# Optimization experiments

Measured on AMD Instinct MI355X. Metric: run time of the kernel, lower is better.

## Reference

```python
import jax, jax.numpy as jnp
import numpy as np

EMBED_DIM = 256
NUM_EMBEDDINGS = 1024
COMMITMENT_COST = 0.25


def setup_inputs() -> dict:
    key = jax.random.key(0)
    k1, k2 = jax.random.split(key)
    z_e = jax.random.normal(k1, (64, 32, 32, EMBED_DIM), dtype=jnp.float32)
    # variance_scaling(fan_in, uniform) ~ U(-sqrt(3/fan_in), sqrt(3/fan_in))
    lim = float(np.sqrt(3.0 / EMBED_DIM))
    codebook = jax.random.uniform(k2, (NUM_EMBEDDINGS, EMBED_DIM), dtype=jnp.float32,
                                  minval=-lim, maxval=lim)
    return {"z_e": z_e, "codebook": codebook}


def reference(z_e, codebook):
    codebook = jnp.asarray(codebook, dtype=jnp.float32)
    z_flat = jnp.reshape(z_e, (-1, codebook.shape[1]))  # [N, D]
    # ||z||^2 - 2 z.c + ||c||^2 -> [N, K]
    distances = (jnp.sum(z_flat ** 2, axis=1, keepdims=True)
                 - 2.0 * jnp.dot(z_flat, codebook.T)
                 + jnp.sum(codebook ** 2, axis=1))
    encoding_indices = jnp.argmin(distances, axis=1)  # [N]
    quantized = jnp.reshape(codebook[encoding_indices], z_e.shape)
    commitment_loss = COMMITMENT_COST * jnp.mean((jax.lax.stop_gradient(quantized) - z_e) ** 2)
    embedding_loss = jnp.mean((quantized - jax.lax.stop_gradient(z_e)) ** 2)
    quantized = z_e + jax.lax.stop_gradient(quantized - z_e)  # straight-through
    return (quantized, commitment_loss, embedding_loss, encoding_indices)
```

## Files before the change

kernel.cpp:

```cpp
#include <hip/hip_runtime.h>

#define NROWS  65536
#define DIM    256
#define KCB    1024
#define DELTA  0.012f
#define DELTA2 2.0e-4f
#define NRMAX  65536

typedef __attribute__((ext_vector_type(8))) _Float16 v8h;
typedef __attribute__((ext_vector_type(4))) float v4f;
typedef __attribute__((ext_vector_type(4))) int   v4i;

__device__ __forceinline__ unsigned short h16(float x) {
  _Float16 h = (_Float16)x;
  return __builtin_bit_cast(unsigned short, h);
}
__device__ __forceinline__ unsigned pk2h(float a, float b) {
  return (unsigned)h16(a) | ((unsigned)h16(b) << 16);
}
__device__ __forceinline__ v4i pk8h(float4 a, float4 b) {
  v4i r; r.x = (int)pk2h(a.x,a.y); r.y = (int)pk2h(a.z,a.w);
  r.z = (int)pk2h(b.x,b.y); r.w = (int)pk2h(b.z,b.w);
  return r;
}
__device__ __forceinline__ float f16f(float x) { return (float)(_Float16)x; }
__device__ __forceinline__ void gld16(const void* g, void* l) {
  __builtin_amdgcn_global_load_lds(
      (const __attribute__((address_space(1))) unsigned int*)g,
      (__attribute__((address_space(3))) unsigned int*)l, 16, 0, 0);
}

__global__ __launch_bounds__(256) void prep_kernel(const float* __restrict__ cb,
                                                   float* __restrict__ cnorm,
                                                   unsigned short* __restrict__ cbh,
                                                   unsigned short* __restrict__ cbl,
                                                   int* __restrict__ cnt,
                                                   int* __restrict__ cnt2) {
  int g = blockIdx.x * 256 + threadIdx.x;
  if (g == 0) { *cnt = 0; *cnt2 = 0; }
  int k = g >> 2, q = g & 3;
  int nt = k >> 7, c = k & 127;
  const float4* row = reinterpret_cast<const float4*>(cb + (size_t)k * DIM) + q * 16;
  size_t off = (size_t)((nt * 4 + q) * 128 + c) * 64;
  unsigned short* dh = cbh + off;
  unsigned short* dl = cbl + off;
  int xr = (c & 7) << 3;
  double s = 0.0;
#pragma unroll
  for (int i = 0; i < 8; ++i) {
    float4 a = row[2 * i], b = row[2 * i + 1];
    s += (double)a.x * a.x + (double)a.y * a.y + (double)a.z * a.z + (double)a.w * a.w;
    s += (double)b.x * b.x + (double)b.y * b.y + (double)b.z * b.z + (double)b.w * b.w;
    *(v4i*)(dh + ((i * 8) ^ xr)) = pk8h(a, b);
    float4 ar, br;
    ar.x = a.x - f16f(a.x); ar.y = a.y - f16f(a.y);
    ar.z = a.z - f16f(a.z); ar.w = a.w - f16f(a.w);
    br.x = b.x - f16f(b.x); br.y = b.y - f16f(b.y);
    br.z = b.z - f16f(b.z); br.w = b.w - f16f(b.w);
    *(v4i*)(dl + ((i * 8) ^ xr)) = pk8h(ar, br);
  }
  s += __shfl_xor(s, 1);
  s += __shfl_xor(s, 2);
  if (q == 0) cnorm[k] = (float)s;
}

__global__ __launch_bounds__(256, 2) void vq_mfma(
    const float* __restrict__ z, const unsigned short* __restrict__ cbh,
    const float* __restrict__ cnw, int* __restrict__ idx_arr,
    int* __restrict__ list, int* __restrict__ cnt) {
  __shared__ __align__(16) short S[32768];

  const int t = threadIdx.x;
  const int l = t & 63;
  const int w = t >> 6;
  const int l15 = l & 15, lhi = l >> 4;
  const int wm = w * 32;
  const int r0 = blockIdx.x * 128;

#pragma unroll
  for (int p = 0; p < 16; ++p) {
    int u = t + p * 256;
    int row = u >> 5, k8 = u & 31;
    const float4* s = (const float4*)(z + (size_t)(r0 + row) * DIM + k8 * 8);
    float4 a = s[0], b = s[1];
    *(v4i*)(S + row * 256 + ((k8 * 8) ^ ((row & 7) << 3))) = pk8h(a, b);
  }
  __syncthreads();

  v8h A[2][8];
#pragma unroll
  for (int mf = 0; mf < 2; ++mf) {
    int arow = wm + mf * 16 + l15;
    int base = arow * 256, xr = (arow & 7) << 3;
#pragma unroll
    for (int ks8 = 0; ks8 < 8; ++ks8)
      A[mf][ks8] = *(const v8h*)(S + base + ((ks8 * 32 + lhi * 8) ^ xr));
  }
  float cn4[4];
#pragma unroll
  for (int j = 0; j < 4; ++j) cn4[j] = cnw[t + j * 256];
  __syncthreads();

  float* CNS = (float*)(S + 24576);
#pragma unroll
  for (int j = 0; j < 4; ++j) CNS[t + j * 256] = cn4[j];

  auto stageC = [&](int g) {
    const char* gb = (const char*)cbh + (size_t)g * 16384 + w * 4096 + l * 16;
    char* lb = (char*)S + (g % 3) * 16384 + w * 4096 + l * 16;
#pragma unroll
    for (int j = 0; j < 4; ++j) gld16(gb + j * 1024, lb + j * 1024);
  };

  int bcode[8], boff[8], bxr[8];
#pragma unroll
  for (int nf = 0; nf < 8; ++nf) {
    bcode[nf] = nf * 16 + l15;
    boff[nf] = bcode[nf] * 64;
    bxr[nf] = (bcode[nf] & 7) << 3;
  }

  float m1[8], m2[8]; int i1[8];
#pragma unroll
  for (int sl = 0; sl < 8; ++sl) { m1[sl] = 3.0e38f; m2[sl] = 3.0e38f; i1[sl] = 0; }

  __syncthreads();
  stageC(0); stageC(1);

  v4f acc[2][8];

  for (int nt = 0; nt < 8; ++nt) {
#pragma unroll
    for (int mf = 0; mf < 2; ++mf)
#pragma unroll
      for (int nf = 0; nf < 8; ++nf) acc[mf][nf] = (v4f){0.f, 0.f, 0.f, 0.f};

    for (int kc = 0; kc < 4; ++kc) {
      int g = nt * 4 + kc;
      if (g < 31) asm volatile("s_waitcnt vmcnt(4)" ::: "memory");
      else        asm volatile("s_waitcnt vmcnt(0)" ::: "memory");
      __builtin_amdgcn_s_barrier();
      __builtin_amdgcn_sched_barrier(0);
      if (g + 2 < 32) stageC(g + 2);
      const short* cur = S + (g % 3) * 8192;
#pragma unroll
      for (int ks = 0; ks < 2; ++ks) {
        int ko = ks * 32 + lhi * 8;
        v8h b[8];
#pragma unroll
        for (int nf = 0; nf < 8; ++nf)
          b[nf] = *(const v8h*)(cur + boff[nf] + (ko ^ bxr[nf]));
#pragma unroll
        for (int mf = 0; mf < 2; ++mf)
#pragma unroll
          for (int nf = 0; nf < 8; ++nf)
            acc[mf][nf] = __builtin_amdgcn_mfma_f32_16x16x32_f16(A[mf][kc * 2 + ks], b[nf], acc[mf][nf], 0, 0, 0);
      }
    }

#pragma unroll
    for (int mf = 0; mf < 2; ++mf)
#pragma unroll
      for (int nf = 0; nf < 8; ++nf) {
        int code = nt * 128 + bcode[nf];
        float cn = CNS[nt * 128 + bcode[nf]];
#pragma unroll
        for (int r = 0; r < 4; ++r) {
          float s = fmaf(-2.f, acc[mf][nf][r], cn);
          int sl = mf * 4 + r;
          m2[sl] = fminf(m2[sl], fmaxf(m1[sl], s));
          bool lt = s < m1[sl];
          i1[sl] = lt ? code : i1[sl];
          m1[sl] = lt ? s : m1[sl];
        }
      }
  }

#pragma unroll
  for (int off = 1; off < 16; off <<= 1) {
#pragma unroll
    for (int sl = 0; sl < 8; ++sl) {
      float o1 = __shfl_xor(m1[sl], off);
      int   oi = __shfl_xor(i1[sl], off);
      float o2 = __shfl_xor(m2[sl], off);
      bool bb = (o1 < m1[sl]) || (o1 == m1[sl] && oi < i1[sl]);
      float hi = fmaxf(m1[sl], o1);
      m2[sl] = fminf(hi, fminf(m2[sl], o2));
      m1[sl] = bb ? o1 : m1[sl];
      i1[sl] = bb ? oi : i1[sl];
    }
  }

  if (l15 == 0) {
#pragma unroll
    for (int sl = 0; sl < 8; ++sl) {
      int row = wm + (sl >> 2) * 16 + lhi * 4 + (sl & 3);
      idx_arr[r0 + row] = i1[sl];
      if (m2[sl] - m1[sl] < DELTA) {
        int p = atomicAdd(cnt, 1);
        list[p] = r0 + row;
      }
    }
  }
}

__global__ __launch_bounds__(256, 1) void vq_refine(
    const float* __restrict__ z,
    const unsigned short* __restrict__ cbh, const unsigned short* __restrict__ cbl,
    const float* __restrict__ cnw, const int* __restrict__ list,
    const int* __restrict__ cnt,
    float* __restrict__ pm1, float* __restrict__ pm2, int* __restrict__ pi1) {
  __shared__ __align__(16) short Ch[2][8192];
  __shared__ __align__(16) short Cl[2][8192];
  __shared__ int rows_s[64];

  const int t = threadIdx.x;
  const int l = t & 63, w = t >> 6;
  const int l15 = l & 15, lhi = l >> 4;
  const int n = *cnt;
  const int ngroups = (n + 63) >> 6;
  const int cq = blockIdx.x & 3;

  auto stage2 = [&](int g, int buf) {
    size_t go = (size_t)g * 16384 + w * 4096 + l * 16;
    char* lh = (char*)Ch[buf] + w * 4096;
    char* ll = (char*)Cl[buf] + w * 4096;
#pragma unroll
    for (int j = 0; j < 4; ++j) gld16((const char*)cbh + go + j * 1024, lh + j * 1024);
#pragma unroll
    for (int j = 0; j < 4; ++j) gld16((const char*)cbl + go + j * 1024, ll + j * 1024);
  };

  const int bxr = (l15 & 7) << 3;

  for (int grp = blockIdx.x >> 2; grp < ngroups; grp += (gridDim.x >> 2)) {
    int base = grp * 64;
    __syncthreads();
    if (t < 64) rows_s[t] = list[min(base + t, n - 1)];
    __syncthreads();
    int rowg = rows_s[w * 16 + l15];

    v8h Ah[8], Al[8];
#pragma unroll
    for (int ks8 = 0; ks8 < 8; ++ks8) {
      const float* p = z + (size_t)rowg * 256 + ks8 * 32 + lhi * 8;
      float4 a = *(const float4*)p, b = *(const float4*)(p + 4);
      v8h hv, lv;
      hv[0] = (_Float16)a.x; lv[0] = (_Float16)(a.x - (float)hv[0]);
      hv[1] = (_Float16)a.y; lv[1] = (_Float16)(a.y - (float)hv[1]);
      hv[2] = (_Float16)a.z; lv[2] = (_Float16)(a.z - (float)hv[2]);
      hv[3] = (_Float16)a.w; lv[3] = (_Float16)(a.w - (float)hv[3]);
      hv[4] = (_Float16)b.x; lv[4] = (_Float16)(b.x - (float)hv[4]);
      hv[5] = (_Float16)b.y; lv[5] = (_Float16)(b.y - (float)hv[5]);
      hv[6] = (_Float16)b.z; lv[6] = (_Float16)(b.z - (float)hv[6]);
      hv[7] = (_Float16)b.w; lv[7] = (_Float16)(b.w - (float)hv[7]);
      Ah[ks8] = hv; Al[ks8] = lv;
    }

    stage2(cq * 8, 0);
    __syncthreads();

    float m1[4], m2[4]; int i1[4];
#pragma unroll
    for (int r = 0; r < 4; ++r) { m1[r] = 3.0e38f; m2[r] = 3.0e38f; i1[r] = 0; }

#pragma unroll
    for (int tnt = 0; tnt < 2; ++tnt) {
      int nt = cq * 2 + tnt;
      float cnv[8];
#pragma unroll
      for (int nf = 0; nf < 8; ++nf) cnv[nf] = cnw[nt * 128 + nf * 16 + l15];

      v4f acc[8];
#pragma unroll
      for (int nf = 0; nf < 8; ++nf) acc[nf] = (v4f){0.f, 0.f, 0.f, 0.f};

      for (int kc = 0; kc < 4; ++kc) {
        int ph = tnt * 4 + kc;
        int g = nt * 4 + kc;
        if (ph < 7) stage2(g + 1, (ph + 1) & 1);
        const short* ch = Ch[ph & 1];
        const short* cl = Cl[ph & 1];
#pragma unroll
        for (int ks = 0; ks < 2; ++ks) {
          int ko = (ks * 32 + lhi * 8) ^ bxr;
          v8h bh[8], bl8[8];
#pragma unroll
          for (int nf = 0; nf < 8; ++nf) {
            int bo = (nf * 16 + l15) * 64 + ko;
            bh[nf]  = *(const v8h*)(ch + bo);
            bl8[nf] = *(const v8h*)(cl + bo);
          }
          v8h ah = Ah[kc * 2 + ks], al = Al[kc * 2 + ks];
#pragma unroll
          for (int nf = 0; nf < 8; ++nf) {
            acc[nf] = __builtin_amdgcn_mfma_f32_16x16x32_f16(al, bh[nf], acc[nf], 0, 0, 0);
            acc[nf] = __builtin_amdgcn_mfma_f32_16x16x32_f16(ah, bl8[nf], acc[nf], 0, 0, 0);
            acc[nf] = __builtin_amdgcn_mfma_f32_16x16x32_f16(ah, bh[nf], acc[nf], 0, 0, 0);
          }
        }
        __syncthreads();
      }

#pragma unroll
      for (int nf = 0; nf < 8; ++nf) {
        int code = nt * 128 + nf * 16 + l15;
#pragma unroll
        for (int r = 0; r < 4; ++r) {
          float s = fmaf(-2.f, acc[nf][r], cnv[nf]);
          m2[r] = fminf(m2[r], fmaxf(m1[r], s));
          bool lt = s < m1[r];
          i1[r] = lt ? code : i1[r];
          m1[r] = lt ? s : m1[r];
        }
      }
    }

#pragma unroll
    for (int off = 1; off < 16; off <<= 1) {
#pragma unroll
      for (int r = 0; r < 4; ++r) {
        float o1 = __shfl_xor(m1[r], off);
        int   oi = __shfl_xor(i1[r], off);
        float o2 = __shfl_xor(m2[r], off);
        bool bb = (o1 < m1[r]) || (o1 == m1[r] && oi < i1[r]);
        float hi = fmaxf(m1[r], o1);
        m2[r] = fminf(hi, fminf(m2[r], o2));
        m1[r] = bb ? o1 : m1[r];
        i1[r] = bb ? oi : i1[r];
      }
    }

    if (l15 == 0) {
#pragma unroll
      for (int r = 0; r < 4; ++r) {
        int fr = w * 16 + lhi * 4 + r;
        int pos = base + fr;
        if (pos < n) {
          pm1[cq * NRMAX + pos] = m1[r];
          pm2[cq * NRMAX + pos] = m2[r];
          pi1[cq * NRMAX + pos] = i1[r];
        }
      }
    }
  }
}

__global__ __launch_bounds__(256) void vq_merge(
    const int* __restrict__ list, const int* __restrict__ cnt,
    const float* __restrict__ pm1, const float* __restrict__ pm2,
    const int* __restrict__ pi1, int* __restrict__ idx_arr,
    int* __restrict__ list2, int* __restrict__ cnt2) {
  int i = blockIdx.x * 256 + threadIdx.x;
  int n = *cnt;
  if (i >= n) return;
  float m1 = pm1[i], m2 = pm2[i];
  int   i1 = pi1[i];
#pragma unroll
  for (int cq = 1; cq < 4; ++cq) {
    float o1 = pm1[cq * NRMAX + i];
    float o2 = pm2[cq * NRMAX + i];
    int   oi = pi1[cq * NRMAX + i];
    bool bb = (o1 < m1) || (o1 == m1 && oi < i1);
    float hi = fmaxf(m1, o1);
    m2 = fminf(hi, fminf(m2, o2));
    m1 = bb ? o1 : m1;
    i1 = bb ? oi : i1;
  }
  int row = list[i];
  idx_arr[row] = i1;
  if (m2 - m1 < DELTA2) {
    int p = atomicAdd(cnt2, 1);
    list2[p] = row;
  }
}

__global__ __launch_bounds__(256) void vq_rescue(
    const float* __restrict__ z, const float* __restrict__ cb,
    const float* __restrict__ cnw, const int* __restrict__ list,
    const int* __restrict__ cnt, int* __restrict__ idx_arr) {
  __shared__ float zs[256];
  __shared__ float As;
  __shared__ float wmin[4];
  __shared__ int   widx[4];

  const int t = threadIdx.x;
  const int l = t & 63, w = t >> 6;
  const int n = *cnt;

  for (int i = blockIdx.x; i < n; i += gridDim.x) {
    int row = list[i];
    __syncthreads();
    if (t < 64) ((float4*)zs)[t] = ((const float4*)(z + (size_t)row * DIM))[t];
    __syncthreads();
    if (t < 4) {
      double s = 0.0;
      const float* zz = zs + t * 64;
      for (int d = 0; d < 64; ++d) { float v = zz[d]; s += (double)v * v; }
      s += __shfl_xor(s, 1);
      s += __shfl_xor(s, 2);
      if (t == 0) As = (float)s;
    }
    __syncthreads();
    float Af = As;

    const float4* c0 = (const float4*)(cb + (size_t)(t      ) * DIM);
    const float4* c1 = (const float4*)(cb + (size_t)(t + 256) * DIM);
    const float4* c2 = (const float4*)(cb + (size_t)(t + 512) * DIM);
    const float4* c3 = (const float4*)(cb + (size_t)(t + 768) * DIM);
    float a0 = 0.f, a1 = 0.f, a2 = 0.f, a3 = 0.f;
    for (int d4 = 0; d4 < 64; ++d4) {
      float4 zq = *(const float4*)(zs + d4 * 4);
      float4 va = c0[d4], vb = c1[d4], vc = c2[d4], vd = c3[d4];
      a0 = fmaf(zq.x, va.x, a0); a0 = fmaf(zq.y, va.y, a0);
      a0 = fmaf(zq.z, va.z, a0); a0 = fmaf(zq.w, va.w, a0);
      a1 = fmaf(zq.x, vb.x, a1); a1 = fmaf(zq.y, vb.y, a1);
      a1 = fmaf(zq.z, vb.z, a1); a1 = fmaf(zq.w, vb.w, a1);
      a2 = fmaf(zq.x, vc.x, a2); a2 = fmaf(zq.y, vc.y, a2);
      a2 = fmaf(zq.z, vc.z, a2); a2 = fmaf(zq.w, vc.w, a2);
      a3 = fmaf(zq.x, vd.x, a3); a3 = fmaf(zq.y, vd.y, a3);
      a3 = fmaf(zq.z, vd.z, a3); a3 = fmaf(zq.w, vd.w, a3);
    }
    float accs[4] = {a0, a1, a2, a3};
    float mv = 3.0e38f; int mi = 0;
#pragma unroll
    for (int j = 0; j < 4; ++j) {
      int code = t + j * 256;
      float t1 = fmaf(-2.f, accs[j], Af);
      float t2 = t1 + cnw[code];
      if (t2 < mv) { mv = t2; mi = code; }
    }
#pragma unroll
    for (int off = 1; off < 64; off <<= 1) {
      float ov = __shfl_xor(mv, off);
      int   oi = __shfl_xor(mi, off);
      if (ov < mv || (ov == mv && oi < mi)) { mv = ov; mi = oi; }
    }
    if (l == 0) { wmin[w] = mv; widx[w] = mi; }
    __syncthreads();
    if (t == 0) {
      float bm = wmin[0]; int bi = widx[0];
#pragma unroll
      for (int q = 1; q < 4; ++q)
        if (wmin[q] < bm || (wmin[q] == bm && widx[q] < bi)) { bm = wmin[q]; bi = widx[q]; }
      idx_arr[row] = bi;
    }
    __syncthreads();
  }
}

__global__ __launch_bounds__(256) void vq_epilogue(
    const float* __restrict__ z, const float* __restrict__ cb,
    const int* __restrict__ idx_arr, float* __restrict__ out_q,
    float* __restrict__ out_idx, double* __restrict__ partial) {
  __shared__ int idxs[16];
  __shared__ double lw[4];
  const int t = threadIdx.x;
  const int b0 = blockIdx.x * 16;
  if (t < 16) {
    int k = idx_arr[b0 + t];
    idxs[t] = k;
    out_idx[b0 + t] = (float)k;
  }
  __syncthreads();
  const float4* zb = (const float4*)(z + (size_t)b0 * DIM);
  float4* qb = (float4*)(out_q + (size_t)b0 * DIM);
  double ls = 0.0;
#pragma unroll
  for (int p = 0; p < 4; ++p) {
    int fi = p * 256 + t;
    int ki = idxs[fi >> 6];
    float4 zv = zb[fi];
    float4 cv = ((const float4*)(cb + (size_t)ki * DIM))[fi & 63];
    float dx = cv.x - zv.x, dy = cv.y - zv.y, dz = cv.z - zv.z, dw = cv.w - zv.w;
    float4 o; o.x = zv.x + dx; o.y = zv.y + dy; o.z = zv.z + dz; o.w = zv.w + dw;
    qb[fi] = o;
    ls += (double)dx * dx + (double)dy * dy + (double)dz * dz + (double)dw * dw;
  }
#pragma unroll
  for (int off = 1; off < 64; off <<= 1) ls += __shfl_xor(ls, off);
  if ((t & 63) == 0) lw[t >> 6] = ls;
  __syncthreads();
  if (t == 0) partial[blockIdx.x] = lw[0] + lw[1] + lw[2] + lw[3];
}

__global__ __launch_bounds__(256) void finalize_kernel(const double* __restrict__ partial,
                                                       float* __restrict__ out_losses) {
  __shared__ double lw[4];
  const int t = threadIdx.x;
  double s = 0.0;
  for (int i = t; i < 4096; i += 256) s += partial[i];
#pragma unroll
  for (int off = 1; off < 64; off <<= 1) s += __shfl_xor(s, off);
  if ((t & 63) == 0) lw[t >> 6] = s;
  __syncthreads();
  if (t == 0) {
    double mse = (lw[0] + lw[1] + lw[2] + lw[3]) / ((double)NROWS * (double)DIM);
    out_losses[0] = (float)(0.25 * mse);
    out_losses[1] = (float)mse;
  }
}

extern "C" void kernel_launch(void* const* d_in, const int* in_sizes, int n_in,
                              void* d_out, int out_size, void* d_ws, size_t ws_size,
                              hipStream_t stream) {
  const float* z  = (const float*)d_in[0];
  const float* cb = (const float*)d_in[1];
  float* out = (float*)d_out;

  char* ws = (char*)d_ws;
  int*            cnt     = (int*)(ws + 0);
  int*            cnt2    = (int*)(ws + 8);
  float*          cnorm   = (float*)(ws + 4096);
  double*         partial = (double*)(ws + 8192);
  int*            idx_arr = (int*)(ws + 40960);
  int*            list    = (int*)(ws + 303104);
  int*            list2   = (int*)(ws + 565248);
  unsigned short* cbh     = (unsigned short*)(ws + 827392);
  unsigned short* cbl     = (unsigned short*)(ws + 1351680);
  float*          pm1     = (float*)(ws + 1875968);
  float*          pm2     = (float*)(ws + 2924544);
  int*            pi1     = (int*)(ws + 3973120);

  float* out_q      = out;
  float* out_losses = out + 16777216;
  float* out_idx    = out + 16777218;

  prep_kernel<<<16, 256, 0, stream>>>(cb, cnorm, cbh, cbl, cnt, cnt2);
  vq_mfma<<<NROWS / 128, 256, 0, stream>>>(z, cbh, cnorm, idx_arr, list, cnt);
  vq_refine<<<1024, 256, 0, stream>>>(z, cbh, cbl, cnorm, list, cnt, pm1, pm2, pi1);
  vq_merge<<<NRMAX / 256, 256, 0, stream>>>(list, cnt, pm1, pm2, pi1, idx_arr, list2, cnt2);
  vq_rescue<<<256, 256, 0, stream>>>(z, cb, cnorm, list2, cnt2, idx_arr);
  vq_epilogue<<<NROWS / 16, 256, 0, stream>>>(z, cb, idx_arr, out_q, out_idx, partial);
  finalize_kernel<<<1, 256, 0, stream>>>(partial, out_losses);
}
```

Measured before the change: 146.1 us.

## Load z fragments directly to registers and double-buffer codebook tiles in LDS

The query tile is now converted to fp16 straight from global memory into MFMA A-fragments, which removes the LDS staging pass and its two barriers. Codebook norms are read from global memory instead of an LDS copy. The codebook pipeline drops from triple buffering with explicit vmcnt waits to double buffering with a flat 32-step loop and a __syncthreads per step. This halves LDS use and simplifies the schedule, but it cuts prefetch depth and adds full barriers each step, which may expose load latency.

```diff
diff --git a/kernel.cpp b/kernel.cpp
--- a/kernel.cpp
+++ b/kernel.cpp
@@ -68,7 +68,7 @@
     const float* __restrict__ z, const unsigned short* __restrict__ cbh,
     const float* __restrict__ cnw, int* __restrict__ idx_arr,
     int* __restrict__ list, int* __restrict__ cnt) {
-  __shared__ __align__(16) short S[32768];
+  __shared__ __align__(16) short Cs[2][8192];
 
   const int t = threadIdx.x;
   const int l = t & 63;
@@ -77,37 +77,26 @@
   const int wm = w * 32;
   const int r0 = blockIdx.x * 128;
 
-#pragma unroll
-  for (int p = 0; p < 16; ++p) {
-    int u = t + p * 256;
-    int row = u >> 5, k8 = u & 31;
-    const float4* s = (const float4*)(z + (size_t)(r0 + row) * DIM + k8 * 8);
-    float4 a = s[0], b = s[1];
-    *(v4i*)(S + row * 256 + ((k8 * 8) ^ ((row & 7) << 3))) = pk8h(a, b);
-  }
-  __syncthreads();
-
   v8h A[2][8];
 #pragma unroll
   for (int mf = 0; mf < 2; ++mf) {
-    int arow = wm + mf * 16 + l15;
-    int base = arow * 256, xr = (arow & 7) << 3;
-#pragma unroll
-    for (int ks8 = 0; ks8 < 8; ++ks8)
-      A[mf][ks8] = *(const v8h*)(S + base + ((ks8 * 32 + lhi * 8) ^ xr));
-  }
-  float cn4[4];
-#pragma unroll
-  for (int j = 0; j < 4; ++j) cn4[j] = cnw[t + j * 256];
-  __syncthreads();
-
-  float* CNS = (float*)(S + 24576);
-#pragma unroll
-  for (int j = 0; j < 4; ++j) CNS[t + j * 256] = cn4[j];
+    const float* zr = z + (size_t)(r0 + wm + mf * 16 + l15) * DIM;
+#pragma unroll
+    for (int ks8 = 0; ks8 < 8; ++ks8) {
+      const float* p = zr + ks8 * 32 + lhi * 8;
+      float4 a = *(const float4*)p, b = *(const float4*)(p + 4);
+      v8h hv;
+      hv[0] = (_Float16)a.x; hv[1] = (_Float16)a.y;
+      hv[2] = (_Float16)a.z; hv[3] = (_Float16)a.w;
+      hv[4] = (_Float16)b.x; hv[5] = (_Float16)b.y;
+      hv[6] = (_Float16)b.z; hv[7] = (_Float16)b.w;
+      A[mf][ks8] = hv;
+    }
+  }
 
   auto stageC = [&](int g) {
     const char* gb = (const char*)cbh + (size_t)g * 16384 + w * 4096 + l * 16;
-    char* lb = (char*)S + (g % 3) * 16384 + w * 4096 + l * 16;
+    char* lb = (char*)Cs[g & 1] + w * 4096;
 #pragma unroll
     for (int j = 0; j < 4; ++j) gld16(gb + j * 1024, lb + j * 1024);
   };
@@ -124,56 +113,54 @@
 #pragma unroll
   for (int sl = 0; sl < 8; ++sl) { m1[sl] = 3.0e38f; m2[sl] = 3.0e38f; i1[sl] = 0; }
 
+  v4f acc[2][8];
+
+  stageC(0);
   __syncthreads();
-  stageC(0); stageC(1);
-
-  v4f acc[2][8];
-
-  for (int nt = 0; nt < 8; ++nt) {
-#pragma unroll
-    for (int mf = 0; mf < 2; ++mf)
-#pragma unroll
-      for (int nf = 0; nf < 8; ++nf) acc[mf][nf] = (v4f){0.f, 0.f, 0.f, 0.f};
-
-    for (int kc = 0; kc < 4; ++kc) {
-      int g = nt * 4 + kc;
-      if (g < 31) asm volatile("s_waitcnt vmcnt(4)" ::: "memory");
-      else        asm volatile("s_waitcnt vmcnt(0)" ::: "memory");
-      __builtin_amdgcn_s_barrier();
-      __builtin_amdgcn_sched_barrier(0);
-      if (g + 2 < 32) stageC(g + 2);
-      const short* cur = S + (g % 3) * 8192;
-#pragma unroll
-      for (int ks = 0; ks < 2; ++ks) {
-        int ko = ks * 32 + lhi * 8;
-        v8h b[8];
+
+  for (int g = 0; g < 32; ++g) {
+    if (g < 31) stageC(g + 1);
+    const int kc = g & 3;
+    if (kc == 0) {
+#pragma unroll
+      for (int mf = 0; mf < 2; ++mf)
+#pragma unroll
+        for (int nf = 0; nf < 8; ++nf) acc[mf][nf] = (v4f){0.f, 0.f, 0.f, 0.f};
+    }
+    const short* cur = Cs[g & 1];
+#pragma unroll
+    for (int ks = 0; ks < 2; ++ks) {
+      int ko = ks * 32 + lhi * 8;
+      v8h b[8];
+#pragma unroll
+      for (int nf = 0; nf < 8; ++nf)
+        b[nf] = *(const v8h*)(cur + boff[nf] + (ko ^ bxr[nf]));
+#pragma unroll
+      for (int mf = 0; mf < 2; ++mf)
 #pragma unroll
         for (int nf = 0; nf < 8; ++nf)
-          b[nf] = *(const v8h*)(cur + boff[nf] + (ko ^ bxr[nf]));
-#pragma unroll
-        for (int mf = 0; mf < 2; ++mf)
-#pragma unroll
-          for (int nf = 0; nf < 8; ++nf)
-            acc[mf][nf] = __builtin_amdgcn_mfma_f32_16x16x32_f16(A[mf][kc * 2 + ks], b[nf], acc[mf][nf], 0, 0, 0);
-      }
-    }
-
-#pragma unroll
-    for (int mf = 0; mf < 2; ++mf)
-#pragma unroll
-      for (int nf = 0; nf < 8; ++nf) {
-        int code = nt * 128 + bcode[nf];
-        float cn = CNS[nt * 128 + bcode[nf]];
-#pragma unroll
-        for (int r = 0; r < 4; ++r) {
-          float s = fmaf(-2.f, acc[mf][nf][r], cn);
-          int sl = mf * 4 + r;
-          m2[sl] = fminf(m2[sl], fmaxf(m1[sl], s));
-          bool lt = s < m1[sl];
-          i1[sl] = lt ? code : i1[sl];
-          m1[sl] = lt ? s : m1[sl];
+          acc[mf][nf] = __builtin_amdgcn_mfma_f32_16x16x32_f16(A[mf][kc * 2 + ks], b[nf], acc[mf][nf], 0, 0, 0);
+    }
+    if (kc == 3) {
+      int nt = g >> 2;
+#pragma unroll
+      for (int mf = 0; mf < 2; ++mf)
+#pragma unroll
+        for (int nf = 0; nf < 8; ++nf) {
+          int code = nt * 128 + bcode[nf];
+          float cn = cnw[code];
+#pragma unroll
+          for (int r = 0; r < 4; ++r) {
+            float s = fmaf(-2.f, acc[mf][nf][r], cn);
+            int sl = mf * 4 + r;
+            m2[sl] = fminf(m2[sl], fmaxf(m1[sl], s));
+            bool lt = s < m1[sl];
+            i1[sl] = lt ? code : i1[sl];
+            m1[sl] = lt ? s : m1[sl];
+          }
         }
-      }
+    }
+    __syncthreads();
   }
 
 #pragma unroll
```

New measurement: 177.9 us. +21.8%, slower.
